# Kernel tuning notes

Measured on AMD Instinct MI355X. Metric: run time of the kernel, lower is better.

The kernel has to match this reference:

```python
import jax, jax.numpy as jnp
import numpy as np
from jax import lax

STRIDES = (8, 16, 32)
NUM_CLASSES = 80
TOPK = 1000
CONF_THRESH = 0.05
NMS_THRESH = 0.6


def setup_inputs() -> dict:
    key = jax.random.key(0)
    ks = jax.random.split(key, 10)
    hw = [(256, 256), (128, 128), (64, 64)]
    inp = {}
    for lv, (h, w) in enumerate(hw):
        inp[f"cls_pred_{lv}"] = jax.random.normal(ks[3 * lv + 0], (NUM_CLASSES, h, w), jnp.float32)
        inp[f"reg_pred_{lv}"] = jax.random.normal(ks[3 * lv + 1], (4, h, w), jnp.float32)
        inp[f"ctn_pred_{lv}"] = jax.random.normal(ks[3 * lv + 2], (1, h, w), jnp.float32)
    inp["scales"] = jax.random.uniform(ks[9], (3,), jnp.float32)
    return inp


def _level_decode(cls_p, reg_p, ctn_p, scale, stride):
    # cls_p: [C,H,W] -> flatten to [M,C] matching torch permute(1,2,0).view(-1,C)
    C, H, W = cls_p.shape
    cls = jnp.transpose(cls_p, (1, 2, 0)).reshape(-1, C)          # [M,C]
    reg = jnp.transpose(reg_p, (1, 2, 0)).reshape(-1, 4)          # [M,4]
    reg = jax.nn.relu(reg * scale) * stride                       # Scale + relu + stride
    ctn = jnp.transpose(ctn_p, (1, 2, 0)).reshape(-1, 1)          # [M,1]
    joint = jnp.sqrt(jax.nn.sigmooid(cls) * jax.nn.sigmoid(ctn)) if False else \
        jnp.sqrt(jax.nn.sigmoid(cls) * jax.nn.sigmoid(ctn))      # [M,C]
    scores = jnp.max(joint, axis=-1)                              # [M]
    labels = jnp.argmax(joint, axis=-1)                           # [M]
    ay, ax = jnp.meshgrid(jnp.arange(H), jnp.arange(W), indexing='ij')
    anchors = (jnp.stack([ax, ay], -1).reshape(-1, 2).astype(cls.dtype) + 0.5) * stride  # [M,2]
    # per-level topk (M > TOPK for all levels here)
    scores, idx = lax.top_k(scores, TOPK)
    labels = labels[idx]
    reg = reg[idx]
    anchors = anchors[idx]
    boxes = jnp.concatenate([anchors - reg[:, :2], anchors + reg[:, 2:]], axis=-1)  # x1y1x2y2
    return scores, labels, boxes


def _nms(boxes, scores):
    # Faithful port of the pure-python NMS: fixed-shape keep mask, sorted order.
    N = boxes.shape[0]
    order = jnp.argsort(-scores)
    b = boxes[order]
    x1, y1, x2, y2 = b[:, 0], b[:, 1], b[:, 2], b[:, 3]
    areas = (x2 - x1) * (y2 - y1)
    xx1 = jnp.maximum(x1[:, None], x1[None, :])
    yy1 = jnp.maximum(y1[:, None], y1[None, :])
    xx2 = jnp.minimum(x2[:, None], x2[None, :])
    yy2 = jnp.minimum(y2[:, None], y2[None, :])
    w = jnp.maximum(1e-10, xx2 - xx1)
    h = jnp.maximum(1e-10, yy2 - yy1)
    inter = w * h
    iou = inter / (areas[:, None] + areas[None, :] - inter + 1e-14)  # [N,N]
    idxs = jnp.arange(N)

    def body(i, keep):
        sup = (iou[i] > NMS_THRESH) & (idxs > i) & keep[i]
        return keep & ~sup

    keep = lax.fori_loop(0, N, body, jnp.ones((N,), bool))
    return order, keep


def reference(cls_pred_0, cls_pred_1, cls_pred_2,
              reg_pred_0, reg_pred_1, reg_pred_2,
              ctn_pred_0, ctn_pred_1, ctn_pred_2, scales):
    cls_l = [cls_pred_0, cls_pred_1, cls_pred_2]
    reg_l = [reg_pred_0, reg_pred_1, reg_pred_2]
    ctn_l = [ctn_pred_0, ctn_pred_1, ctn_pred_2]
    all_s, all_l, all_b = [], [], []
    for lv in range(3):
        s, lb, bx = _level_decode(cls_l[lv], reg_l[lv], ctn_l[lv], scales[lv], float(STRIDES[lv]))
        all_s.append(s); all_l.append(lb); all_b.append(bx)
    scores = jnp.concatenate(all_s)   # [3000]
    labels = jnp.concatenate(all_l)
    boxes = jnp.concatenate(all_b)    # [3000,4]
    order, keep = _nms(boxes, scores)
    scores_s = scores[order]
    labels_s = labels[order]
    boxes_s = boxes[order]
    keep = keep & (scores_s > CONF_THRESH)
    return boxes_s, scores_s, labels_s, keep
```

## Files before the change

kernel.cpp:

```cpp
#include <hip/hip_runtime.h>
#include <cmath>
#include <stdint.h>

#define NPTS   86016
#define NCB    1024
#define K_TOP  1000
#define NOUT   3000
#define NWORDS 47
#define NTILE  47
#define ECAP   8192
#define FCAP   1024
#define SPPB   64

#define CH_OFF     0
#define FINE_OFF   (NCB * 3 * 4)
#define CNT_OFF    (FINE_OFF + 3 * 256 * 4)
#define MEMSET_BYTES (CNT_OFF + 64)
#define KEYS_OFF   (CNT_OFF + 64)
#define LAB_OFF    (KEYS_OFF + NPTS * 8)
#define COMB_OFF   (LAB_OFF + NPTS * 4)
#define SURV_OFF   (COMB_OFF + 3 * 65536 * 8)
#define EDGE_OFF   (SURV_OFF + NOUT * 8 + 64)
#define FLAG_OFF   (EDGE_OFF + ECAP * 4)

__device__ __forceinline__ float sig_f32_stepwise(float x) {
    float e = (float)exp(-(double)x);
    return 1.0f / (1.0f + e);
}

__device__ __forceinline__ void locate(int g, int& lv, int& p, int& HW) {
    if (g < 65536)      { lv = 0; p = g;         HW = 65536; }
    else if (g < 81920) { lv = 1; p = g - 65536; HW = 16384; }
    else                { lv = 2; p = g - 81920; HW = 4096;  }
}

__global__ __launch_bounds__(256) void score_kernel(
        const float* __restrict__ cls0, const float* __restrict__ cls1,
        const float* __restrict__ cls2,
        const float* __restrict__ ctn0, const float* __restrict__ ctn1,
        const float* __restrict__ ctn2,
        unsigned long long* __restrict__ keys, int* __restrict__ labels,
        int* __restrict__ chist,
        int* __restrict__ cnt, unsigned* __restrict__ flags) {
    __shared__ float pm[5 * SPPB], pv[5 * SPPB];
    __shared__ int pidx[5 * SPPB];
    __shared__ int lch[NCB];
    const int tid = threadIdx.x;
    const int base = blockIdx.x * SPPB;
    for (int i = tid; i < NCB; i += 256) lch[i] = 0;
    for (int it = tid; it < 5 * SPPB; it += 256) {
        int c = it / SPPB, pt = it - c * SPPB;
        int g = base + pt, lv, p, HW;
        locate(g, lv, p, HW);
        const float* cls = (lv == 0) ? cls0 : ((lv == 1) ? cls1 : cls2);
        const float* bp = cls + (size_t)c * 16 * HW + p;
        float x[16];
#pragma unroll
        for (int cc = 0; cc < 16; cc++) x[cc] = bp[(size_t)cc * HW];
        float m = -INFINITY, v = -INFINITY; int idx = 0;
#pragma unroll
        for (int cc = 0; cc < 16; cc++)
            if (x[cc] > m) { v = m; m = x[cc]; idx = c * 16 + cc; }
        pm[it] = m; pv[it] = v; pidx[it] = idx;
    }
    __syncthreads();
    if (tid < SPPB) {
        int g = base + tid, lv, p, HW;
        locate(g, lv, p, HW);
        const float* ctn = (lv == 0) ? ctn0 : ((lv == 1) ? ctn1 : ctn2);
        float m = -INFINITY, v = -INFINITY; int idx = 0;
#pragma unroll
        for (int k = 0; k < 5; k++) {
            float bm = pm[k * SPPB + tid];
            float bv = pv[k * SPPB + tid];
            int bidx = pidx[k * SPPB + tid];
            if (bm > m) { v = fmaxf(m, bv); m = bm; idx = bidx; }
        }
        float sc = sig_f32_stepwise(ctn[p]);
        float sM = sig_f32_stepwise(m);
        float jm = __fsqrt_rn(sM * sc);
        float sV = sig_f32_stepwise(v);
        float jv = __fsqrt_rn(sV * sc);
        if (jv == jm) {
            int f = atomicAdd(&cnt[13], 1);
            if (f < FCAP) flags[f] = (unsigned)g;
        }
        unsigned int bits = __float_as_uint(jm);
        keys[g] = ((unsigned long long)bits << 32) | (0xFFFFFFFFu - (unsigned)g);
        labels[g] = idx;
        atomicAdd(&lch[(int)(bits >> 20)], 1);
    }
    __syncthreads();
    int lv0, p0, HW0; locate(base, lv0, p0, HW0);
    for (int i = tid; i < NCB; i += 256) {
        int v = lch[i];
        if (v) atomicAdd(&chist[lv0 * NCB + i], v);
    }
}

__global__ __launch_bounds__(1024) void scan_kernel(
        const unsigned long long* __restrict__ keys,
        const int* __restrict__ chist,
        int* __restrict__ cnt, int* __restrict__ fineg,
        unsigned long long* __restrict__ comb) {
    const int bid = blockIdx.x, tid = threadIdx.x;
    const int lane = tid & 63, wv = tid >> 6;
    const unsigned long long lmlt = (1ULL << lane) - 1;
    int lv, off;
    if (bid < 64)      { lv = 0; off = bid << 10; }
    else if (bid < 80) { lv = 1; off = (bid - 64) << 10; }
    else               { lv = 2; off = (bid - 80) << 10; }
    const int base = (lv == 0) ? 0 : ((lv == 1) ? 65536 : 81920);

    __shared__ int wtot[16], wsuf[16];
    __shared__ int s_chunk;
    __shared__ int lcnt, labove, lbase;
    __shared__ unsigned long long buf[1024];

    if (tid == 0) { lcnt = 0; labove = 0; }
    unsigned long long key = keys[base + off + tid];

    {
        int s = chist[lv * NCB + tid];
#pragma unroll
        for (int o = 1; o <= 32; o <<= 1) {
            int t = __shfl_down(s, o, 64);
            if (lane + o < 64) s += t;
        }
        if (lane == 0) wtot[wv] = s;
        __syncthreads();
        if (tid < 16) {
            int t = wtot[tid];
#pragma unroll
            for (int o = 1; o <= 8; o <<= 1) {
                int q = __shfl_down(t, o, 64);
                if (tid + o < 16) t += q;
            }
            wsuf[tid] = t;
        }
        __syncthreads();
        int offW = (wv < 15) ? wsuf[wv + 1] : 0;
        int part_i = s + offW;
        int s1 = __shfl_down(s, 1, 64);
        int part_n = (lane < 63) ? (s1 + offW) : offW;
        if (part_i >= K_TOP && part_n < K_TOP) s_chunk = tid;
    }
    __syncthreads();
    const int chunk = s_chunk;

    int cb = (int)(key >> 52);
    bool keep = cb >= chunk;
    unsigned long long mK = __ballot(keep);
    if (mK) {
        int ldr = __ffsll((long long)mK) - 1;
        int bk;
        if (lane == ldr) bk = atomicAdd(&lcnt, __popcll(mK));
        bk = __shfl(bk, ldr, 64);
        if (keep) buf[bk + __popcll(mK & lmlt)] = key;
    }
    unsigned long long mS = __ballot(cb > chunk);
    if (lane == 0 && mS) atomicAdd(&labove, __popcll(mS));
    if (cb == chunk)
        atomicAdd(&fineg[lv * 256 + ((int)(key >> 44) & 255)], 1);
    __syncthreads();
    if (tid == 0) {
        lbase = atomicAdd(&cnt[0 + lv], lcnt);
        if (labove) atomicAdd(&cnt[3 + lv], labove);
        cnt[6 + lv] = chunk;
    }
    __syncthreads();
    if (tid < lcnt) comb[(size_t)lv * 65536 + lbase + tid] = buf[tid];
}

__global__ __launch_bounds__(1024) void select_kernel(
        const float* __restrict__ cls0, const float* __restrict__ cls1,
        const float* __restrict__ cls2,
        const float* __restrict__ ctn0, const float* __restrict__ ctn1,
        const float* __restrict__ ctn2,
        const int* __restrict__ cnt, const int* __restrict__ fineg,
        const unsigned long long* __restrict__ comb,
        const unsigned* __restrict__ flags, int* __restrict__ labels,
        unsigned long long* __restrict__ surv) {
    int bid = blockIdx.x, tid = threadIdx.x;
    if (bid == 3) {
        int nf = cnt[13]; if (nf > FCAP) nf = FCAP;
        int wave = tid >> 6, lane = tid & 63;
        for (int f = wave; f < nf; f += 16) {
            int g = (int)flags[f], lv, p, HW;
            locate(g, lv, p, HW);
            const float* cls = (lv == 0) ? cls0 : ((lv == 1) ? cls1 : cls2);
            const float* ctn = (lv == 0) ? ctn0 : ((lv == 1) ? ctn1 : ctn2);
            float sc = sig_f32_stepwise(ctn[p]);
            float bestv = -1.0f; int besti = 127;
            {
                float s = sig_f32_stepwise(cls[(size_t)lane * HW + p]);
                float sj = __fsqrt_rn(s * sc);
                bestv = sj; besti = lane;
            }
            if (lane < 16) {
                int c2 = lane + 64;
                float s = sig_f32_stepwise(cls[(size_t)c2 * HW + p]);
                float sj = __fsqrt_rn(s * sc);
                if (sj > bestv) { bestv = sj; besti = c2; }
            }
            for (int off = 32; off; off >>= 1) {
                float ov = __shfl_xor(bestv, off, 64);
                int   oi = __shfl_xor(besti, off, 64);
                if (ov > bestv || (ov == bestv && oi < besti)) { bestv = ov; besti = oi; }
            }
            if (lane == 0) labels[g] = besti;
        }
        return;
    }
    const int lv = bid;
    const int lane = tid & 63, wv = tid >> 6;
    const unsigned long long lmlt = (1ULL << lane) - 1;
    __shared__ int wtot[16], wsuf[16];
    __shared__ int sBf, sSure, sCand;
    __shared__ unsigned long long sel[1024];
    __shared__ unsigned long long cbuf[1024];

    const int n     = cnt[0 + lv];
    const int above = cnt[3 + lv];
    const int chunk = cnt[6 + lv];
    if (tid == 0) { sSure = 0; sCand = 0; }

    {
        int fs = (tid < 256) ? fineg[lv * 256 + tid] : 0;
#pragma unroll
        for (int o = 1; o <= 32; o <<= 1) {
            int t = __shfl_down(fs, o, 64);
            if (lane + o < 64) fs += t;
        }
        if (tid < 256 && lane == 0) wtot[wv] = fs;
        __syncthreads();
        if (tid < 4) {
            int t = wtot[tid];
#pragma unroll
            for (int o = 1; o <= 2; o <<= 1) {
                int q = __shfl_down(t, o, 64);
                if (tid + o < 4) t += q;
            }
            wsuf[tid] = t;
        }
        __syncthreads();
        if (tid < 256) {
            int offW = (wv < 3) ? wsuf[wv + 1] : 0;
            int ge = above + fs + offW;
            int fs1 = __shfl_down(fs, 1, 64);
            int genxt = above + ((lane < 63) ? (fs1 + offW) : offW);
            if (ge >= K_TOP && genxt < K_TOP) sBf = tid;
        }
    }
    __syncthreads();
    const int Bf = sBf;

    for (int i0 = tid; ; i0 += 1024) {
        bool any = (i0 - tid) < n;
        if (!any) break;
        bool valid = i0 < n;
        unsigned long long key = valid ? comb[(size_t)lv * 65536 + i0] : 0ULL;
        int cb = (int)(key >> 52);
        int fb = (int)(key >> 44) & 255;
        bool pS = valid && (cb > chunk || fb > Bf);
        bool pC = valid && (cb == chunk && fb == Bf);
        unsigned long long mS = __ballot(pS);
        if (mS) {
            int ldr = __ffsll((long long)mS) - 1;
            int bk;
            if (lane == ldr) bk = atomicAdd(&sSure, __popcll(mS));
            bk = __shfl(bk, ldr, 64);
            if (pS) sel[bk + __popcll(mS & lmlt)] = key;
        }
        unsigned long long mC = __ballot(pC);
        if (mC) {
            int ldr = __ffsll((long long)mC) - 1;
            int bk;
            if (lane == ldr) bk = atomicAdd(&sCand, __popcll(mC));
            bk = __shfl(bk, ldr, 64);
            if (pC) {
                int pos = bk + __popcll(mC & lmlt);
                if (pos < 1024) cbuf[pos] = key;
            }
        }
    }
    __syncthreads();

    const int nS = sSure;
    int nC = sCand; if (nC > 1024) nC = 1024;
    unsigned long long myS = (tid < nS) ? sel[tid] : 0ULL;
    unsigned long long myC = (tid < nC) ? cbuf[tid] : 0ULL;
    int a0 = 0, a1 = 0, a2 = 0, a3 = 0;
    int i = 0;
    for (; i + 4 <= nS; i += 4) {
        a0 += (sel[i] > myS); a1 += (sel[i + 1] > myS);
        a2 += (sel[i + 2] > myS); a3 += (sel[i + 3] > myS);
    }
    for (; i < nS; i++) a0 += (sel[i] > myS);
    int rS = a0 + a1 + a2 + a3;
    int b0 = 0, b1 = 0, b2 = 0, b3 = 0;
    i = 0;
    for (; i + 4 <= nC; i += 4) {
        b0 += (cbuf[i] > myC); b1 += (cbuf[i + 1] > myC);
        b2 += (cbuf[i + 2] > myC); b3 += (cbuf[i + 3] > myC);
    }
    for (; i < nC; i++) b0 += (cbuf[i] > myC);
    int rC = b0 + b1 + b2 + b3;
    __syncthreads();
    if (tid < nS) sel[rS] = myS;
    if (tid < nC) cbuf[rC] = myC;
    __syncthreads();
    if (tid < K_TOP) surv[lv * K_TOP + tid] = (tid < nS) ? sel[tid] : cbuf[tid - nS];
}

__global__ __launch_bounds__(1024) void merge_emit_kernel(
        const unsigned long long* __restrict__ surv,
        const int* __restrict__ labels,
        const float* __restrict__ reg0, const float* __restrict__ reg1,
        const float* __restrict__ reg2,
        const float* __restrict__ scales,
        float* __restrict__ out) {
    __shared__ unsigned long long L[3][1024];
    __shared__ unsigned long long s[NOUT];
    int tid = threadIdx.x;
#pragma unroll
    for (int lv = 0; lv < 3; lv++)
        L[lv][tid] = (tid < K_TOP) ? surv[lv * K_TOP + tid] : 0ULL;
    __syncthreads();
    for (int e = tid; e < NOUT; e += 1024) {
        int a = e / K_TOP, i = e - a * K_TOP;
        unsigned long long key = L[a][i];
        int rank = i;
#pragma unroll
        for (int b = 0; b < 3; b++) {
            if (b == a) continue;
            int lo = 0, hi = K_TOP;
            while (lo < hi) {
                int mid = (lo + hi) >> 1;
                if (L[b][mid] > key) lo = mid + 1; else hi = mid;
            }
            rank += lo;
        }
        s[rank] = key;
    }
    __syncthreads();
    for (int r = tid; r < NOUT; r += 1024) {
        unsigned long long key = s[r];
        unsigned int bits = (unsigned)(key >> 32);
        float score = __uint_as_float(bits);
        unsigned int g = 0xFFFFFFFFu - (unsigned)(key & 0xFFFFFFFFULL);
        int lv, p;
        if (g < 65536u)      { lv = 0; p = (int)g; }
        else if (g < 81920u) { lv = 1; p = (int)g - 65536; }
        else                 { lv = 2; p = (int)g - 81920; }
        const float* rp = (lv == 0) ? reg0 : ((lv == 1) ? reg1 : reg2);
        int HW = (lv == 0) ? 65536 : ((lv == 1) ? 16384 : 4096);
        int W = 256 >> lv;
        float strideF = (float)(8 << lv);
        float scale = scales[lv];
        int x = p & (W - 1);
        int y = p >> (8 - lv);
        float r0 = fmaxf(0.0f, rp[0 * HW + p] * scale) * strideF;
        float r1 = fmaxf(0.0f, rp[1 * HW + p] * scale) * strideF;
        float r2 = fmaxf(0.0f, rp[2 * HW + p] * scale) * strideF;
        float r3 = fmaxf(0.0f, rp[3 * HW + p] * scale) * strideF;
        float ax = ((float)x + 0.5f) * strideF;
        float ay = ((float)y + 0.5f) * strideF;
        out[r * 4 + 0] = ax - r0;
        out[r * 4 + 1] = ay - r1;
        out[r * 4 + 2] = ax + r2;
        out[r * 4 + 3] = ay + r3;
        out[12000 + r] = score;
        out[15000 + r] = (float)labels[g];
    }
}

__global__ __launch_bounds__(256) void edge_kernel(const float* __restrict__ out,
                                                   unsigned* __restrict__ edges_g,
                                                   int* __restrict__ cnt) {
    __shared__ float x1[128], y1[128], x2[128], y2[128];
    int t = blockIdx.x, tid = threadIdx.x;
    int ta = 0, rem = t;
    while (rem >= NTILE - ta) { rem -= NTILE - ta; ta++; }
    int tb = ta + rem;
    if (tid < 64) {
        int gi = ta * 64 + tid;
        if (gi < NOUT) {
            float4 b = ((const float4*)out)[gi];
            x1[tid] = b.x; y1[tid] = b.y; x2[tid] = b.z; y2[tid] = b.w;
        }
    } else if (tid < 128) {
        int gj = tb * 64 + (tid - 64);
        if (gj < NOUT) {
            float4 b = ((const float4*)out)[gj];
            x1[tid] = b.x; y1[tid] = b.y; x2[tid] = b.z; y2[tid] = b.w;
        }
    }
    __syncthreads();
#pragma unroll
    for (int q = 0; q < 16; q++) {
        int idx = q * 256 + tid;
        int ii = idx >> 6, jj = idx & 63;
        int i = ta * 64 + ii, j = tb * 64 + jj;
        if (i < j && j < NOUT) {
            float ai = (x2[ii] - x1[ii]) * (y2[ii] - y1[ii]);
            float aj = (x2[64 + jj] - x1[64 + jj]) * (y2[64 + jj] - y1[64 + jj]);
            float xx1 = fmaxf(x1[ii], x1[64 + jj]), yy1 = fmaxf(y1[ii], y1[64 + jj]);
            float xx2 = fminf(x2[ii], x2[64 + jj]), yy2 = fminf(y2[ii], y2[64 + jj]);
            float ww = fmaxf(1e-10f, xx2 - xx1);
            float hh = fmaxf(1e-10f, yy2 - yy1);
            float inter = ww * hh;
            float iou = inter / (((ai + aj) - inter) + 1e-14f);
            if ((double)iou > 0.6) {
                int e = atomicAdd(&cnt[12], 1);
                if (e < ECAP) edges_g[e] = ((unsigned)i << 12) | (unsigned)j;
            }
        }
    }
}

__global__ __launch_bounds__(1024) void nms_sparse_kernel(
        const unsigned* __restrict__ edges_g,
        const int* __restrict__ cnt,
        const float* __restrict__ scores_s,
        float* __restrict__ keep_out) {
    __shared__ unsigned ed[ECAP];
    __shared__ unsigned long long supLds[NWORDS];
    int tid = threadIdx.x;
    int E = cnt[12]; if (E > ECAP) E = ECAP;
    int m = 1; while (m < E) m <<= 1;
    for (int t = tid; t < m; t += 1024) ed[t] = (t < E) ? edges_g[t] : 0xFFFFFFFFu;
    __syncthreads();
    for (int k = 2; k <= m; k <<= 1)
        for (int j = k >> 1; j > 0; j >>= 1) {
            for (int t = tid; t < m; t += 1024) {
                int l = t ^ j;
                if (l > t) {
                    unsigned a = ed[t], b = ed[l];
                    if (((t & k) == 0) ? (a > b) : (a < b)) { ed[t] = b; ed[l] = a; }
                }
            }
            __syncthreads();
        }
    if (tid < 64) {
        int lane = tid;
        unsigned long long supW = 0ULL;
        int ep = 0;
        for (int c = 0; c < NWORDS; c++) {
            unsigned long long cw = __shfl(supW, c, 64);
            int hi = (c + 1) * 64;
            while (ep < E) {
                unsigned k = ed[ep];
                int i = (int)(k >> 12);
                if (i >= hi) break;
                int j = (int)(k & 4095);
                if (!((cw >> (i & 63)) & 1ULL)) {
                    if ((j >> 6) == c) cw |= 1ULL << (j & 63);
                    else if (lane == (j >> 6)) supW |= 1ULL << (j & 63);
                }
                ep++;
            }
            if (lane == c) supW = cw;
        }
        if (lane < NWORDS) supLds[lane] = supW;
    }
    __syncthreads();
    for (int j = tid; j < NOUT; j += 1024) {
        bool s = (supLds[j >> 6] >> (j & 63)) & 1ULL;
        float scv = scores_s[j];
        keep_out[j] = (!s && ((double)scv > 0.05)) ? 1.0f : 0.0f;
    }
}

extern "C" void kernel_launch(void* const* d_in, const int* in_sizes, int n_in,
                              void* d_out, int out_size, void* d_ws, size_t ws_size,
                              hipStream_t stream) {
    const float* cls0 = (const float*)d_in[0];
    const float* reg0 = (const float*)d_in[1];
    const float* ctn0 = (const float*)d_in[2];
    const float* cls1 = (const float*)d_in[3];
    const float* reg1 = (const float*)d_in[4];
    const float* ctn1 = (const float*)d_in[5];
    const float* cls2 = (const float*)d_in[6];
    const float* reg2 = (const float*)d_in[7];
    const float* ctn2 = (const float*)d_in[8];
    const float* scales = (const float*)d_in[9];

    char* ws = (char*)d_ws;
    int* chist = (int*)(ws + CH_OFF);
    int* fineg = (int*)(ws + FINE_OFF);
    int* cnt  = (int*)(ws + CNT_OFF);
    unsigned long long* keys = (unsigned long long*)(ws + KEYS_OFF);
    int* labels = (int*)(ws + LAB_OFF);
    unsigned long long* comb = (unsigned long long*)(ws + COMB_OFF);
    unsigned long long* surv = (unsigned long long*)(ws + SURV_OFF);
    unsigned* edges = (unsigned*)(ws + EDGE_OFF);
    unsigned* flags = (unsigned*)(ws + FLAG_OFF);
    float* out = (float*)d_out;

    hipMemsetAsync(ws, 0, MEMSET_BYTES, stream);

    score_kernel<<<NPTS / SPPB, 256, 0, stream>>>(cls0, cls1, cls2, ctn0, ctn1, ctn2,
                                                  keys, labels, chist, cnt, flags);
    scan_kernel<<<84, 1024, 0, stream>>>(keys, chist, cnt, fineg, comb);
    select_kernel<<<4, 1024, 0, stream>>>(cls0, cls1, cls2, ctn0, ctn1, ctn2,
                                          cnt, fineg, comb, flags, labels, surv);
    merge_emit_kernel<<<1, 1024, 0, stream>>>(surv, labels, reg0, reg1, reg2, scales, out);
    edge_kernel<<<NTILE * (NTILE + 1) / 2, 256, 0, stream>>>(out, edges, cnt);
    nms_sparse_kernel<<<1, 1024, 0, stream>>>(edges, cnt, out + 12000, out + 18000);
}
```

Baseline: 167.3 us.

## Fuse pipeline stages via last-block-done atomics to cut kernel launches

Merges the six-kernel pipeline into three kernels. The last block to finish (detected with a threadfence and an atomic counter) runs the follow-on stage: the flag-cleanup pass moves into score_kernel, per-level select and the merge/emit move into the scan kernel, and the sparse NMS moves into the edge kernel. Shared memory is reused through unions. This removes launch gaps and inter-kernel drains. In exchange, the serial tail stages now run in a single block, with fewer threads for the cleanup (256 instead of 1024) and for the NMS bitonic sort, and the scan blocks carry a larger shared-memory footprint.

```diff
diff --git a/kernel.cpp b/kernel.cpp
--- a/kernel.cpp
+++ b/kernel.cpp
@@ -8,6 +8,7 @@
 #define NOUT   3000
 #define NWORDS 47
 #define NTILE  47
+#define NTILES (NTILE * (NTILE + 1) / 2)
 #define ECAP   8192
 #define FCAP   1024
 #define SPPB   64
@@ -15,8 +16,8 @@
 #define CH_OFF     0
 #define FINE_OFF   (NCB * 3 * 4)
 #define CNT_OFF    (FINE_OFF + 3 * 256 * 4)
-#define MEMSET_BYTES (CNT_OFF + 64)
-#define KEYS_OFF   (CNT_OFF + 64)
+#define MEMSET_BYTES (CNT_OFF + 128)
+#define KEYS_OFF   (CNT_OFF + 128)
 #define LAB_OFF    (KEYS_OFF + NPTS * 8)
 #define COMB_OFF   (LAB_OFF + NPTS * 4)
 #define SURV_OFF   (COMB_OFF + 3 * 65536 * 8)
@@ -45,6 +46,7 @@
     __shared__ float pm[5 * SPPB], pv[5 * SPPB];
     __shared__ int pidx[5 * SPPB];
     __shared__ int lch[NCB];
+    __shared__ int doClean;
     const int tid = threadIdx.x;
     const int base = blockIdx.x * SPPB;
     for (int i = tid; i < NCB; i += 256) lch[i] = 0;
@@ -96,96 +98,19 @@
         int v = lch[i];
         if (v) atomicAdd(&chist[lv0 * NCB + i], v);
     }
-}
-
-__global__ __launch_bounds__(1024) void scan_kernel(
-        const unsigned long long* __restrict__ keys,
-        const int* __restrict__ chist,
-        int* __restrict__ cnt, int* __restrict__ fineg,
-        unsigned long long* __restrict__ comb) {
-    const int bid = blockIdx.x, tid = threadIdx.x;
-    const int lane = tid & 63, wv = tid >> 6;
-    const unsigned long long lmlt = (1ULL << lane) - 1;
-    int lv, off;
-    if (bid < 64)      { lv = 0; off = bid << 10; }
-    else if (bid < 80) { lv = 1; off = (bid - 64) << 10; }
-    else               { lv = 2; off = (bid - 80) << 10; }
-    const int base = (lv == 0) ? 0 : ((lv == 1) ? 65536 : 81920);
-
-    __shared__ int wtot[16], wsuf[16];
-    __shared__ int s_chunk;
-    __shared__ int lcnt, labove, lbase;
-    __shared__ unsigned long long buf[1024];
-
-    if (tid == 0) { lcnt = 0; labove = 0; }
-    unsigned long long key = keys[base + off + tid];
-
-    {
-        int s = chist[lv * NCB + tid];
-#pragma unroll
-        for (int o = 1; o <= 32; o <<= 1) {
-            int t = __shfl_down(s, o, 64);
-            if (lane + o < 64) s += t;
-        }
-        if (lane == 0) wtot[wv] = s;
-        __syncthreads();
-        if (tid < 16) {
-            int t = wtot[tid];
-#pragma unroll
-            for (int o = 1; o <= 8; o <<= 1) {
-                int q = __shfl_down(t, o, 64);
-                if (tid + o < 16) t += q;
-            }
-            wsuf[tid] = t;
-        }
-        __syncthreads();
-        int offW = (wv < 15) ? wsuf[wv + 1] : 0;
-        int part_i = s + offW;
-        int s1 = __shfl_down(s, 1, 64);
-        int part_n = (lane < 63) ? (s1 + offW) : offW;
-        if (part_i >= K_TOP && part_n < K_TOP) s_chunk = tid;
-    }
-    __syncthreads();
-    const int chunk = s_chunk;
-
-    int cb = (int)(key >> 52);
-    bool keep = cb >= chunk;
-    unsigned long long mK = __ballot(keep);
-    if (mK) {
-        int ldr = __ffsll((long long)mK) - 1;
-        int bk;
-        if (lane == ldr) bk = atomicAdd(&lcnt, __popcll(mK));
-        bk = __shfl(bk, ldr, 64);
-        if (keep) buf[bk + __popcll(mK & lmlt)] = key;
-    }
-    unsigned long long mS = __ballot(cb > chunk);
-    if (lane == 0 && mS) atomicAdd(&labove, __popcll(mS));
-    if (cb == chunk)
-        atomicAdd(&fineg[lv * 256 + ((int)(key >> 44) & 255)], 1);
     __syncthreads();
     if (tid == 0) {
-        lbase = atomicAdd(&cnt[0 + lv], lcnt);
-        if (labove) atomicAdd(&cnt[3 + lv], labove);
-        cnt[6 + lv] = chunk;
-    }
-    __syncthreads();
-    if (tid < lcnt) comb[(size_t)lv * 65536 + lbase + tid] = buf[tid];
-}
-
-__global__ __launch_bounds__(1024) void select_kernel(
-        const float* __restrict__ cls0, const float* __restrict__ cls1,
-        const float* __restrict__ cls2,
-        const float* __restrict__ ctn0, const float* __restrict__ ctn1,
-        const float* __restrict__ ctn2,
-        const int* __restrict__ cnt, const int* __restrict__ fineg,
-        const unsigned long long* __restrict__ comb,
-        const unsigned* __restrict__ flags, int* __restrict__ labels,
-        unsigned long long* __restrict__ surv) {
-    int bid = blockIdx.x, tid = threadIdx.x;
-    if (bid == 3) {
+        __threadfence();
+        int prev = atomicAdd(&cnt[14], 1);
+        int dc = (prev == (int)gridDim.x - 1);
+        if (dc) __threadfence();
+        doClean = dc;
+    }
+    __syncthreads();
+    if (doClean) {
         int nf = cnt[13]; if (nf > FCAP) nf = FCAP;
         int wave = tid >> 6, lane = tid & 63;
-        for (int f = wave; f < nf; f += 16) {
+        for (int f = wave; f < nf; f += 4) {
             int g = (int)flags[f], lv, p, HW;
             locate(g, lv, p, HW);
             const float* cls = (lv == 0) ? cls0 : ((lv == 1) ? cls1 : cls2);
@@ -210,175 +135,269 @@
             }
             if (lane == 0) labels[g] = besti;
         }
-        return;
-    }
-    const int lv = bid;
-    const int lane = tid & 63, wv = tid >> 6;
-    const unsigned long long lmlt = (1ULL << lane) - 1;
-    __shared__ int wtot[16], wsuf[16];
-    __shared__ int sBf, sSure, sCand;
-    __shared__ unsigned long long sel[1024];
-    __shared__ unsigned long long cbuf[1024];
-
-    const int n     = cnt[0 + lv];
-    const int above = cnt[3 + lv];
-    const int chunk = cnt[6 + lv];
-    if (tid == 0) { sSure = 0; sCand = 0; }
-
-    {
-        int fs = (tid < 256) ? fineg[lv * 256 + tid] : 0;
-#pragma unroll
-        for (int o = 1; o <= 32; o <<= 1) {
-            int t = __shfl_down(fs, o, 64);
-            if (lane + o < 64) fs += t;
-        }
-        if (tid < 256 && lane == 0) wtot[wv] = fs;
-        __syncthreads();
-        if (tid < 4) {
-            int t = wtot[tid];
-#pragma unroll
-            for (int o = 1; o <= 2; o <<= 1) {
-                int q = __shfl_down(t, o, 64);
-                if (tid + o < 4) t += q;
-            }
-            wsuf[tid] = t;
-        }
-        __syncthreads();
-        if (tid < 256) {
-            int offW = (wv < 3) ? wsuf[wv + 1] : 0;
-            int ge = above + fs + offW;
-            int fs1 = __shfl_down(fs, 1, 64);
-            int genxt = above + ((lane < 63) ? (fs1 + offW) : offW);
-            if (ge >= K_TOP && genxt < K_TOP) sBf = tid;
-        }
-    }
-    __syncthreads();
-    const int Bf = sBf;
-
-    for (int i0 = tid; ; i0 += 1024) {
-        bool any = (i0 - tid) < n;
-        if (!any) break;
-        bool valid = i0 < n;
-        unsigned long long key = valid ? comb[(size_t)lv * 65536 + i0] : 0ULL;
-        int cb = (int)(key >> 52);
-        int fb = (int)(key >> 44) & 255;
-        bool pS = valid && (cb > chunk || fb > Bf);
-        bool pC = valid && (cb == chunk && fb == Bf);
-        unsigned long long mS = __ballot(pS);
-        if (mS) {
-            int ldr = __ffsll((long long)mS) - 1;
-            int bk;
-            if (lane == ldr) bk = atomicAdd(&sSure, __popcll(mS));
-            bk = __shfl(bk, ldr, 64);
-            if (pS) sel[bk + __popcll(mS & lmlt)] = key;
-        }
-        unsigned long long mC = __ballot(pC);
-        if (mC) {
-            int ldr = __ffsll((long long)mC) - 1;
-            int bk;
-            if (lane == ldr) bk = atomicAdd(&sCand, __popcll(mC));
-            bk = __shfl(bk, ldr, 64);
-            if (pC) {
-                int pos = bk + __popcll(mC & lmlt);
-                if (pos < 1024) cbuf[pos] = key;
-            }
-        }
-    }
-    __syncthreads();
-
-    const int nS = sSure;
-    int nC = sCand; if (nC > 1024) nC = 1024;
-    unsigned long long myS = (tid < nS) ? sel[tid] : 0ULL;
-    unsigned long long myC = (tid < nC) ? cbuf[tid] : 0ULL;
-    int a0 = 0, a1 = 0, a2 = 0, a3 = 0;
-    int i = 0;
-    for (; i + 4 <= nS; i += 4) {
-        a0 += (sel[i] > myS); a1 += (sel[i + 1] > myS);
-        a2 += (sel[i + 2] > myS); a3 += (sel[i + 3] > myS);
-    }
-    for (; i < nS; i++) a0 += (sel[i] > myS);
-    int rS = a0 + a1 + a2 + a3;
-    int b0 = 0, b1 = 0, b2 = 0, b3 = 0;
-    i = 0;
-    for (; i + 4 <= nC; i += 4) {
-        b0 += (cbuf[i] > myC); b1 += (cbuf[i + 1] > myC);
-        b2 += (cbuf[i + 2] > myC); b3 += (cbuf[i + 3] > myC);
-    }
-    for (; i < nC; i++) b0 += (cbuf[i] > myC);
-    int rC = b0 + b1 + b2 + b3;
-    __syncthreads();
-    if (tid < nS) sel[rS] = myS;
-    if (tid < nC) cbuf[rC] = myC;
-    __syncthreads();
-    if (tid < K_TOP) surv[lv * K_TOP + tid] = (tid < nS) ? sel[tid] : cbuf[tid - nS];
+    }
 }
 
-__global__ __launch_bounds__(1024) void merge_emit_kernel(
-        const unsigned long long* __restrict__ surv,
+__global__ __launch_bounds__(1024) void scansel_kernel(
+        const unsigned long long* __restrict__ keys,
+        const int* __restrict__ chist,
+        int* __restrict__ cnt, int* __restrict__ fineg,
+        unsigned long long* __restrict__ comb,
+        unsigned long long* __restrict__ surv,
         const int* __restrict__ labels,
         const float* __restrict__ reg0, const float* __restrict__ reg1,
         const float* __restrict__ reg2,
         const float* __restrict__ scales,
         float* __restrict__ out) {
-    __shared__ unsigned long long L[3][1024];
-    __shared__ unsigned long long s[NOUT];
-    int tid = threadIdx.x;
-#pragma unroll
-    for (int lv = 0; lv < 3; lv++)
-        L[lv][tid] = (tid < K_TOP) ? surv[lv * K_TOP + tid] : 0ULL;
-    __syncthreads();
-    for (int e = tid; e < NOUT; e += 1024) {
-        int a = e / K_TOP, i = e - a * K_TOP;
-        unsigned long long key = L[a][i];
-        int rank = i;
-#pragma unroll
-        for (int b = 0; b < 3; b++) {
-            if (b == a) continue;
-            int lo = 0, hi = K_TOP;
-            while (lo < hi) {
-                int mid = (lo + hi) >> 1;
-                if (L[b][mid] > key) lo = mid + 1; else hi = mid;
-            }
-            rank += lo;
-        }
-        s[rank] = key;
-    }
-    __syncthreads();
-    for (int r = tid; r < NOUT; r += 1024) {
-        unsigned long long key = s[r];
-        unsigned int bits = (unsigned)(key >> 32);
-        float score = __uint_as_float(bits);
-        unsigned int g = 0xFFFFFFFFu - (unsigned)(key & 0xFFFFFFFFULL);
-        int lv, p;
-        if (g < 65536u)      { lv = 0; p = (int)g; }
-        else if (g < 81920u) { lv = 1; p = (int)g - 65536; }
-        else                 { lv = 2; p = (int)g - 81920; }
-        const float* rp = (lv == 0) ? reg0 : ((lv == 1) ? reg1 : reg2);
-        int HW = (lv == 0) ? 65536 : ((lv == 1) ? 16384 : 4096);
-        int W = 256 >> lv;
-        float strideF = (float)(8 << lv);
-        float scale = scales[lv];
-        int x = p & (W - 1);
-        int y = p >> (8 - lv);
-        float r0 = fmaxf(0.0f, rp[0 * HW + p] * scale) * strideF;
-        float r1 = fmaxf(0.0f, rp[1 * HW + p] * scale) * strideF;
-        float r2 = fmaxf(0.0f, rp[2 * HW + p] * scale) * strideF;
-        float r3 = fmaxf(0.0f, rp[3 * HW + p] * scale) * strideF;
-        float ax = ((float)x + 0.5f) * strideF;
-        float ay = ((float)y + 0.5f) * strideF;
-        out[r * 4 + 0] = ax - r0;
-        out[r * 4 + 1] = ay - r1;
-        out[r * 4 + 2] = ax + r2;
-        out[r * 4 + 3] = ay + r3;
-        out[12000 + r] = score;
-        out[15000 + r] = (float)labels[g];
+    const int bid = blockIdx.x, tid = threadIdx.x;
+    const int lane = tid & 63, wv = tid >> 6;
+    const unsigned long long lmlt = (1ULL << lane) - 1;
+    int lv, off, nblk_lv;
+    if (bid < 64)      { lv = 0; off = bid << 10;        nblk_lv = 64; }
+    else if (bid < 80) { lv = 1; off = (bid - 64) << 10; nblk_lv = 16; }
+    else               { lv = 2; off = (bid - 80) << 10; nblk_lv = 4;  }
+    const int base = (lv == 0) ? 0 : ((lv == 1) ? 65536 : 81920);
+
+    __shared__ int wtot[16], wsuf[16];
+    __shared__ int s_chunk;
+    __shared__ int lcnt, labove, lbase;
+    __shared__ int doSel, doMerge;
+    __shared__ int sBf, sSure, sCand;
+    __shared__ union {
+        unsigned long long buf[1024];
+        struct { unsigned long long sel[1024], cbuf[1024]; } se;
+        struct { unsigned long long L[3][1024], s[NOUT]; } mg;
+    } u;
+
+    if (tid == 0) { lcnt = 0; labove = 0; doMerge = 0; }
+    unsigned long long key = keys[base + off + tid];
+
+    {
+        int s = chist[lv * NCB + tid];
+#pragma unroll
+        for (int o = 1; o <= 32; o <<= 1) {
+            int t = __shfl_down(s, o, 64);
+            if (lane + o < 64) s += t;
+        }
+        if (lane == 0) wtot[wv] = s;
+        __syncthreads();
+        if (tid < 16) {
+            int t = wtot[tid];
+#pragma unroll
+            for (int o = 1; o <= 8; o <<= 1) {
+                int q = __shfl_down(t, o, 64);
+                if (tid + o < 16) t += q;
+            }
+            wsuf[tid] = t;
+        }
+        __syncthreads();
+        int offW = (wv < 15) ? wsuf[wv + 1] : 0;
+        int part_i = s + offW;
+        int s1 = __shfl_down(s, 1, 64);
+        int part_n = (lane < 63) ? (s1 + offW) : offW;
+        if (part_i >= K_TOP && part_n < K_TOP) s_chunk = tid;
+    }
+    __syncthreads();
+    const int chunk = s_chunk;
+
+    {
+        int cb = (int)(key >> 52);
+        bool keep = cb >= chunk;
+        unsigned long long mK = __ballot(keep);
+        if (mK) {
+            int ldr = __ffsll((long long)mK) - 1;
+            int bk;
+            if (lane == ldr) bk = atomicAdd(&lcnt, __popcll(mK));
+            bk = __shfl(bk, ldr, 64);
+            if (keep) u.buf[bk + __popcll(mK & lmlt)] = key;
+        }
+        unsigned long long mS = __ballot(cb > chunk);
+        if (lane == 0 && mS) atomicAdd(&labove, __popcll(mS));
+        if (cb == chunk)
+            atomicAdd(&fineg[lv * 256 + ((int)(key >> 44) & 255)], 1);
+    }
+    __syncthreads();
+    if (tid == 0) {
+        lbase = atomicAdd(&cnt[0 + lv], lcnt);
+        if (labove) atomicAdd(&cnt[3 + lv], labove);
+    }
+    __syncthreads();
+    if (tid < lcnt) comb[(size_t)lv * 65536 + lbase + tid] = u.buf[tid];
+
+    __syncthreads();
+    if (tid == 0) {
+        __threadfence();
+        int prev = atomicAdd(&cnt[9 + lv], 1);
+        int ds = (prev == nblk_lv - 1);
+        if (ds) __threadfence();
+        doSel = ds;
+    }
+    __syncthreads();
+    if (doSel) {
+        const int n     = cnt[0 + lv];
+        const int above = cnt[3 + lv];
+        if (tid == 0) { sSure = 0; sCand = 0; }
+        {
+            int fs = (tid < 256) ? fineg[lv * 256 + tid] : 0;
+#pragma unroll
+            for (int o = 1; o <= 32; o <<= 1) {
+                int t = __shfl_down(fs, o, 64);
+                if (lane + o < 64) fs += t;
+            }
+            if (tid < 256 && lane == 0) wtot[wv] = fs;
+            __syncthreads();
+            if (tid < 4) {
+                int t = wtot[tid];
+#pragma unroll
+                for (int o = 1; o <= 2; o <<= 1) {
+                    int q = __shfl_down(t, o, 64);
+                    if (tid + o < 4) t += q;
+                }
+                wsuf[tid] = t;
+            }
+            __syncthreads();
+            if (tid < 256) {
+                int offW = (wv < 3) ? wsuf[wv + 1] : 0;
+                int ge = above + fs + offW;
+                int fs1 = __shfl_down(fs, 1, 64);
+                int genxt = above + ((lane < 63) ? (fs1 + offW) : offW);
+                if (ge >= K_TOP && genxt < K_TOP) sBf = tid;
+            }
+        }
+        __syncthreads();
+        const int Bf = sBf;
+
+        for (int i0 = tid; ; i0 += 1024) {
+            bool any = (i0 - tid) < n;
+            if (!any) break;
+            bool valid = i0 < n;
+            unsigned long long k2 = valid ? comb[(size_t)lv * 65536 + i0] : 0ULL;
+            int cb = (int)(k2 >> 52);
+            int fb = (int)(k2 >> 44) & 255;
+            bool pS = valid && (cb > chunk || fb > Bf);
+            bool pC = valid && (cb == chunk && fb == Bf);
+            unsigned long long mS = __ballot(pS);
+            if (mS) {
+                int ldr = __ffsll((long long)mS) - 1;
+                int bk;
+                if (lane == ldr) bk = atomicAdd(&sSure, __popcll(mS));
+                bk = __shfl(bk, ldr, 64);
+                if (pS) u.se.sel[bk + __popcll(mS & lmlt)] = k2;
+            }
+            unsigned long long mC = __ballot(pC);
+            if (mC) {
+                int ldr = __ffsll((long long)mC) - 1;
+                int bk;
+                if (lane == ldr) bk = atomicAdd(&sCand, __popcll(mC));
+                bk = __shfl(bk, ldr, 64);
+                if (pC) {
+                    int pos = bk + __popcll(mC & lmlt);
+                    if (pos < 1024) u.se.cbuf[pos] = k2;
+                }
+            }
+        }
+        __syncthreads();
+
+        const int nS = sSure;
+        int nC = sCand; if (nC > 1024) nC = 1024;
+        unsigned long long myS = (tid < nS) ? u.se.sel[tid] : 0ULL;
+        unsigned long long myC = (tid < nC) ? u.se.cbuf[tid] : 0ULL;
+        int a0 = 0, a1 = 0, a2 = 0, a3 = 0;
+        int i = 0;
+        for (; i + 4 <= nS; i += 4) {
+            a0 += (u.se.sel[i] > myS); a1 += (u.se.sel[i + 1] > myS);
+            a2 += (u.se.sel[i + 2] > myS); a3 += (u.se.sel[i + 3] > myS);
+        }
+        for (; i < nS; i++) a0 += (u.se.sel[i] > myS);
+        int rS = a0 + a1 + a2 + a3;
+        int b0 = 0, b1 = 0, b2 = 0, b3 = 0;
+        i = 0;
+        for (; i + 4 <= nC; i += 4) {
+            b0 += (u.se.cbuf[i] > myC); b1 += (u.se.cbuf[i + 1] > myC);
+            b2 += (u.se.cbuf[i + 2] > myC); b3 += (u.se.cbuf[i + 3] > myC);
+        }
+        for (; i < nC; i++) b0 += (u.se.cbuf[i] > myC);
+        int rC = b0 + b1 + b2 + b3;
+        __syncthreads();
+        if (tid < nS) u.se.sel[rS] = myS;
+        if (tid < nC) u.se.cbuf[rC] = myC;
+        __syncthreads();
+        if (tid < K_TOP)
+            surv[lv * K_TOP + tid] = (tid < nS) ? u.se.sel[tid] : u.se.cbuf[tid - nS];
+
+        __syncthreads();
+        if (tid == 0) {
+            __threadfence();
+            int prev = atomicAdd(&cnt[15], 1);
+            int dm = (prev == 2);
+            if (dm) __threadfence();
+            doMerge = dm;
+        }
+    }
+    __syncthreads();
+    if (doMerge) {
+#pragma unroll
+        for (int lv2 = 0; lv2 < 3; lv2++)
+            u.mg.L[lv2][tid] = (tid < K_TOP) ? surv[lv2 * K_TOP + tid] : 0ULL;
+        __syncthreads();
+        for (int e = tid; e < NOUT; e += 1024) {
+            int a = e / K_TOP, i = e - a * K_TOP;
+            unsigned long long k2 = u.mg.L[a][i];
+            int rank = i;
+#pragma unroll
+            for (int b = 0; b < 3; b++) {
+                if (b == a) continue;
+                int lo = 0, hi = K_TOP;
+                while (lo < hi) {
+                    int mid = (lo + hi) >> 1;
+                    if (u.mg.L[b][mid] > k2) lo = mid + 1; else hi = mid;
+                }
+                rank += lo;
+            }
+            u.mg.s[rank] = k2;
+        }
+        __syncthreads();
+        for (int r = tid; r < NOUT; r += 1024) {
+            unsigned long long k2 = u.mg.s[r];
+            unsigned int bits = (unsigned)(k2 >> 32);
+            float score = __uint_as_float(bits);
+            unsigned int g = 0xFFFFFFFFu - (unsigned)(k2 & 0xFFFFFFFFULL);
+            int lv2, p;
+            if (g < 65536u)      { lv2 = 0; p = (int)g; }
+            else if (g < 81920u) { lv2 = 1; p = (int)g - 65536; }
+            else                 { lv2 = 2; p = (int)g - 81920; }
+            const float* rp = (lv2 == 0) ? reg0 : ((lv2 == 1) ? reg1 : reg2);
+            int HW = (lv2 == 0) ? 65536 : ((lv2 == 1) ? 16384 : 4096);
+            int W = 256 >> lv2;
+            float strideF = (float)(8 << lv2);
+            float scale = scales[lv2];
+            int x = p & (W - 1);
+            int y = p >> (8 - lv2);
+            float r0 = fmaxf(0.0f, rp[0 * HW + p] * scale) * strideF;
+            float r1 = fmaxf(0.0f, rp[1 * HW + p] * scale) * strideF;
+            float r2 = fmaxf(0.0f, rp[2 * HW + p] * scale) * strideF;
+            float r3 = fmaxf(0.0f, rp[3 * HW + p] * scale) * strideF;
+            float ax = ((float)x + 0.5f) * strideF;
+            float ay = ((float)y + 0.5f) * strideF;
+            out[r * 4 + 0] = ax - r0;
+            out[r * 4 + 1] = ay - r1;
+            out[r * 4 + 2] = ax + r2;
+            out[r * 4 + 3] = ay + r3;
+            out[12000 + r] = score;
+            out[15000 + r] = (float)labels[g];
+        }
     }
 }
 
-__global__ __launch_bounds__(256) void edge_kernel(const float* __restrict__ out,
-                                                   unsigned* __restrict__ edges_g,
-                                                   int* __restrict__ cnt) {
-    __shared__ float x1[128], y1[128], x2[128], y2[128];
+__global__ __launch_bounds__(256) void edgenms_kernel(
+        float* __restrict__ out,
+        unsigned* __restrict__ edges_g,
+        int* __restrict__ cnt) {
+    __shared__ union {
+        struct { float x1[128], y1[128], x2[128], y2[128]; } eg;
+        struct { unsigned ed[ECAP]; unsigned long long supLds[NWORDS]; } nm;
+    } u;
+    __shared__ int doNms;
     int t = blockIdx.x, tid = threadIdx.x;
     int ta = 0, rem = t;
     while (rem >= NTILE - ta) { rem -= NTILE - ta; ta++; }
@@ -387,13 +406,13 @@
         int gi = ta * 64 + tid;
         if (gi < NOUT) {
             float4 b = ((const float4*)out)[gi];
-            x1[tid] = b.x; y1[tid] = b.y; x2[tid] = b.z; y2[tid] = b.w;
+            u.eg.x1[tid] = b.x; u.eg.y1[tid] = b.y; u.eg.x2[tid] = b.z; u.eg.y2[tid] = b.w;
         }
     } else if (tid < 128) {
         int gj = tb * 64 + (tid - 64);
         if (gj < NOUT) {
             float4 b = ((const float4*)out)[gj];
-            x1[tid] = b.x; y1[tid] = b.y; x2[tid] = b.z; y2[tid] = b.w;
+            u.eg.x1[tid] = b.x; u.eg.y1[tid] = b.y; u.eg.x2[tid] = b.z; u.eg.y2[tid] = b.w;
         }
     }
     __syncthreads();
@@ -403,10 +422,10 @@
         int ii = idx >> 6, jj = idx & 63;
         int i = ta * 64 + ii, j = tb * 64 + jj;
         if (i < j && j < NOUT) {
-            float ai = (x2[ii] - x1[ii]) * (y2[ii] - y1[ii]);
-            float aj = (x2[64 + jj] - x1[64 + jj]) * (y2[64 + jj] - y1[64 + jj]);
-            float xx1 = fmaxf(x1[ii], x1[64 + jj]), yy1 = fmaxf(y1[ii], y1[64 + jj]);
-            float xx2 = fminf(x2[ii], x2[64 + jj]), yy2 = fminf(y2[ii], y2[64 + jj]);
+            float ai = (u.eg.x2[ii] - u.eg.x1[ii]) * (u.eg.y2[ii] - u.eg.y1[ii]);
+            float aj = (u.eg.x2[64 + jj] - u.eg.x1[64 + jj]) * (u.eg.y2[64 + jj] - u.eg.y1[64 + jj]);
+            float xx1 = fmaxf(u.eg.x1[ii], u.eg.x1[64 + jj]), yy1 = fmaxf(u.eg.y1[ii], u.eg.y1[64 + jj]);
+            float xx2 = fminf(u.eg.x2[ii], u.eg.x2[64 + jj]), yy2 = fminf(u.eg.y2[ii], u.eg.y2[64 + jj]);
             float ww = fmaxf(1e-10f, xx2 - xx1);
             float hh = fmaxf(1e-10f, yy2 - yy1);
             float inter = ww * hh;
@@ -417,58 +436,59 @@
             }
         }
     }
-}
-
-__global__ __launch_bounds__(1024) void nms_sparse_kernel(
-        const unsigned* __restrict__ edges_g,
-        const int* __restrict__ cnt,
-        const float* __restrict__ scores_s,
-        float* __restrict__ keep_out) {
-    __shared__ unsigned ed[ECAP];
-    __shared__ unsigned long long supLds[NWORDS];
-    int tid = threadIdx.x;
-    int E = cnt[12]; if (E > ECAP) E = ECAP;
-    int m = 1; while (m < E) m <<= 1;
-    for (int t = tid; t < m; t += 1024) ed[t] = (t < E) ? edges_g[t] : 0xFFFFFFFFu;
-    __syncthreads();
-    for (int k = 2; k <= m; k <<= 1)
-        for (int j = k >> 1; j > 0; j >>= 1) {
-            for (int t = tid; t < m; t += 1024) {
-                int l = t ^ j;
-                if (l > t) {
-                    unsigned a = ed[t], b = ed[l];
-                    if (((t & k) == 0) ? (a > b) : (a < b)) { ed[t] = b; ed[l] = a; }
+    __syncthreads();
+    if (tid == 0) {
+        __threadfence();
+        int prev = atomicAdd(&cnt[16], 1);
+        int dn = (prev == (int)gridDim.x - 1);
+        if (dn) __threadfence();
+        doNms = dn;
+    }
+    __syncthreads();
+    if (doNms) {
+        int E = cnt[12]; if (E > ECAP) E = ECAP;
+        int m = 1; while (m < E) m <<= 1;
+        for (int q = tid; q < m; q += 256) u.nm.ed[q] = (q < E) ? edges_g[q] : 0xFFFFFFFFu;
+        __syncthreads();
+        for (int k = 2; k <= m; k <<= 1)
+            for (int j = k >> 1; j > 0; j >>= 1) {
+                for (int q = tid; q < m; q += 256) {
+                    int l = q ^ j;
+                    if (l > q) {
+                        unsigned a = u.nm.ed[q], b = u.nm.ed[l];
+                        if (((q & k) == 0) ? (a > b) : (a < b)) { u.nm.ed[q] = b; u.nm.ed[l] = a; }
+                    }
                 }
-            }
-            __syncthreads();
-        }
-    if (tid < 64) {
-        int lane = tid;
-        unsigned long long supW = 0ULL;
-        int ep = 0;
-        for (int c = 0; c < NWORDS; c++) {
-            unsigned long long cw = __shfl(supW, c, 64);
-            int hi = (c + 1) * 64;
-            while (ep < E) {
-                unsigned k = ed[ep];
-                int i = (int)(k >> 12);
-                if (i >= hi) break;
-                int j = (int)(k & 4095);
-                if (!((cw >> (i & 63)) & 1ULL)) {
-                    if ((j >> 6) == c) cw |= 1ULL << (j & 63);
-                    else if (lane == (j >> 6)) supW |= 1ULL << (j & 63);
+                __syncthreads();
+            }
+        if (tid < 64) {
+            int lane = tid;
+            unsigned long long supW = 0ULL;
+            int ep = 0;
+            for (int c = 0; c < NWORDS; c++) {
+                unsigned long long cw = __shfl(supW, c, 64);
+                int hi = (c + 1) * 64;
+                while (ep < E) {
+                    unsigned kk = u.nm.ed[ep];
+                    int i = (int)(kk >> 12);
+                    if (i >= hi) break;
+                    int j = (int)(kk & 4095);
+                    if (!((cw >> (i & 63)) & 1ULL)) {
+                        if ((j >> 6) == c) cw |= 1ULL << (j & 63);
+                        else if (lane == (j >> 6)) supW |= 1ULL << (j & 63);
+                    }
+                    ep++;
                 }
-                ep++;
-            }
-            if (lane == c) supW = cw;
-        }
-        if (lane < NWORDS) supLds[lane] = supW;
-    }
-    __syncthreads();
-    for (int j = tid; j < NOUT; j += 1024) {
-        bool s = (supLds[j >> 6] >> (j & 63)) & 1ULL;
-        float scv = scores_s[j];
-        keep_out[j] = (!s && ((double)scv > 0.05)) ? 1.0f : 0.0f;
+                if (lane == c) supW = cw;
+            }
+            if (lane < NWORDS) u.nm.supLds[lane] = supW;
+        }
+        __syncthreads();
+        for (int jj = tid; jj < NOUT; jj += 256) {
+            bool s = (u.nm.supLds[jj >> 6] >> (jj & 63)) & 1ULL;
+            float scv = out[12000 + jj];
+            out[18000 + jj] = (!s && ((double)scv > 0.05)) ? 1.0f : 0.0f;
+        }
     }
 }
 
@@ -502,10 +522,7 @@
 
     score_kernel<<<NPTS / SPPB, 256, 0, stream>>>(cls0, cls1, cls2, ctn0, ctn1, ctn2,
                                                   keys, labels, chist, cnt, flags);
-    scan_kernel<<<84, 1024, 0, stream>>>(keys, chist, cnt, fineg, comb);
-    select_kernel<<<4, 1024, 0, stream>>>(cls0, cls1, cls2, ctn0, ctn1, ctn2,
-                                          cnt, fineg, comb, flags, labels, surv);
-    merge_emit_kernel<<<1, 1024, 0, stream>>>(surv, labels, reg0, reg1, reg2, scales, out);
-    edge_kernel<<<NTILE * (NTILE + 1) / 2, 256, 0, stream>>>(out, edges, cnt);
-    nms_sparse_kernel<<<1, 1024, 0, stream>>>(edges, cnt, out + 12000, out + 18000);
+    scansel_kernel<<<84, 1024, 0, stream>>>(keys, chist, cnt, fineg, comb, surv,
+                                            labels, reg0, reg1, reg2, scales, out);
+    edgenms_kernel<<<NTILES, 256, 0, stream>>>(out, edges, cnt);
 }
```

Result: slower. 213.8 us (+27.8%).

## Restructure score kernel to one wave per block with float4 per-thread class scan

Applied to the files above, without the earlier changes.

The score kernel now assigns four consecutive points to each thread and scans all 80 classes with float4 loads. This replaces the five-way class split that merged partial max/second-max through shared memory. It removes the shared-memory merge, the extra barrier and the per-point level lookup, and it vectorizes global loads. In exchange, far fewer threads are launched (336 single-wave blocks), which may leave the memory system under-occupied and make the read latency-bound.

```diff
diff --git a/kernel.cpp b/kernel.cpp
--- a/kernel.cpp
+++ b/kernel.cpp
@@ -10,7 +10,6 @@
 #define NTILE  47
 #define ECAP   8192
 #define FCAP   1024
-#define SPPB   64
 
 #define CH_OFF     0
 #define FINE_OFF   (NCB * 3 * 4)
@@ -34,7 +33,7 @@
     else                { lv = 2; p = g - 81920; HW = 4096;  }
 }
 
-__global__ __launch_bounds__(256) void score_kernel(
+__global__ __launch_bounds__(64) void score_kernel(
         const float* __restrict__ cls0, const float* __restrict__ cls1,
         const float* __restrict__ cls2,
         const float* __restrict__ ctn0, const float* __restrict__ ctn1,
@@ -42,59 +41,56 @@
         unsigned long long* __restrict__ keys, int* __restrict__ labels,
         int* __restrict__ chist,
         int* __restrict__ cnt, unsigned* __restrict__ flags) {
-    __shared__ float pm[5 * SPPB], pv[5 * SPPB];
-    __shared__ int pidx[5 * SPPB];
     __shared__ int lch[NCB];
     const int tid = threadIdx.x;
-    const int base = blockIdx.x * SPPB;
-    for (int i = tid; i < NCB; i += 256) lch[i] = 0;
-    for (int it = tid; it < 5 * SPPB; it += 256) {
-        int c = it / SPPB, pt = it - c * SPPB;
-        int g = base + pt, lv, p, HW;
-        locate(g, lv, p, HW);
-        const float* cls = (lv == 0) ? cls0 : ((lv == 1) ? cls1 : cls2);
-        const float* bp = cls + (size_t)c * 16 * HW + p;
-        float x[16];
-#pragma unroll
-        for (int cc = 0; cc < 16; cc++) x[cc] = bp[(size_t)cc * HW];
-        float m = -INFINITY, v = -INFINITY; int idx = 0;
-#pragma unroll
-        for (int cc = 0; cc < 16; cc++)
-            if (x[cc] > m) { v = m; m = x[cc]; idx = c * 16 + cc; }
-        pm[it] = m; pv[it] = v; pidx[it] = idx;
-    }
-    __syncthreads();
-    if (tid < SPPB) {
-        int g = base + tid, lv, p, HW;
-        locate(g, lv, p, HW);
-        const float* ctn = (lv == 0) ? ctn0 : ((lv == 1) ? ctn1 : ctn2);
-        float m = -INFINITY, v = -INFINITY; int idx = 0;
-#pragma unroll
-        for (int k = 0; k < 5; k++) {
-            float bm = pm[k * SPPB + tid];
-            float bv = pv[k * SPPB + tid];
-            int bidx = pidx[k * SPPB + tid];
-            if (bm > m) { v = fmaxf(m, bv); m = bm; idx = bidx; }
-        }
-        float sc = sig_f32_stepwise(ctn[p]);
-        float sM = sig_f32_stepwise(m);
-        float jm = __fsqrt_rn(sM * sc);
-        float sV = sig_f32_stepwise(v);
-        float jv = __fsqrt_rn(sV * sc);
+    const int bid = blockIdx.x;
+    int lv, off;
+    if (bid < 256)      { lv = 0; off = bid << 8; }
+    else if (bid < 320) { lv = 1; off = (bid - 256) << 8; }
+    else                { lv = 2; off = (bid - 320) << 8; }
+    const int HW    = (lv == 0) ? 65536 : ((lv == 1) ? 16384 : 4096);
+    const int gbase = (lv == 0) ? 0 : ((lv == 1) ? 65536 : 81920);
+    const float* cls = (lv == 0) ? cls0 : ((lv == 1) ? cls1 : cls2);
+    const float* ctn = (lv == 0) ? ctn0 : ((lv == 1) ? ctn1 : ctn2);
+
+    for (int i = tid; i < NCB; i += 64) lch[i] = 0;
+    __syncthreads();
+
+    const int p = off + (tid << 2);
+    float m[4], v[4]; int ix[4];
+#pragma unroll
+    for (int j = 0; j < 4; j++) { m[j] = -INFINITY; v[j] = -INFINITY; ix[j] = 0; }
+
+#pragma unroll 8
+    for (int cc = 0; cc < 80; cc++) {
+        float4 x4 = *(const float4*)(cls + (size_t)cc * HW + p);
+        float xs[4] = { x4.x, x4.y, x4.z, x4.w };
+#pragma unroll
+        for (int j = 0; j < 4; j++)
+            if (xs[j] > m[j]) { v[j] = m[j]; m[j] = xs[j]; ix[j] = cc; }
+    }
+
+    float4 ct4 = *(const float4*)(ctn + p);
+    float cts[4] = { ct4.x, ct4.y, ct4.z, ct4.w };
+#pragma unroll
+    for (int j = 0; j < 4; j++) {
+        int g = gbase + p + j;
+        float sc = sig_f32_stepwise(cts[j]);
+        float jm = __fsqrt_rn(sig_f32_stepwise(m[j]) * sc);
+        float jv = __fsqrt_rn(sig_f32_stepwise(v[j]) * sc);
         if (jv == jm) {
             int f = atomicAdd(&cnt[13], 1);
             if (f < FCAP) flags[f] = (unsigned)g;
         }
         unsigned int bits = __float_as_uint(jm);
         keys[g] = ((unsigned long long)bits << 32) | (0xFFFFFFFFu - (unsigned)g);
-        labels[g] = idx;
+        labels[g] = ix[j];
         atomicAdd(&lch[(int)(bits >> 20)], 1);
     }
     __syncthreads();
-    int lv0, p0, HW0; locate(base, lv0, p0, HW0);
-    for (int i = tid; i < NCB; i += 256) {
-        int v = lch[i];
-        if (v) atomicAdd(&chist[lv0 * NCB + i], v);
+    for (int i = tid; i < NCB; i += 64) {
+        int vv = lch[i];
+        if (vv) atomicAdd(&chist[lv * NCB + i], vv);
     }
 }
 
@@ -500,8 +496,8 @@
 
     hipMemsetAsync(ws, 0, MEMSET_BYTES, stream);
 
-    score_kernel<<<NPTS / SPPB, 256, 0, stream>>>(cls0, cls1, cls2, ctn0, ctn1, ctn2,
-                                                  keys, labels, chist, cnt, flags);
+    score_kernel<<<336, 64, 0, stream>>>(cls0, cls1, cls2, ctn0, ctn1, ctn2,
+                                         keys, labels, chist, cnt, flags);
     scan_kernel<<<84, 1024, 0, stream>>>(keys, chist, cnt, fineg, comb);
     select_kernel<<<4, 1024, 0, stream>>>(cls0, cls1, cls2, ctn0, ctn1, ctn2,
                                           cnt, fineg, comb, flags, labels, surv);
```

Measured after the change: 164.1 us. No clear change (-1.9%).
